# Performance work log

Hardware: AMD Instinct MI355X
Metric: run time of the kernel (lower is better)

The kernel has to match this reference:

```python
import jax, jax.numpy as jnp
import numpy as np

N_NODES = 100000
N_EDGES = 3200000
N_GRAPHS = 1000
IN_DIM = 10
HIDDEN = 64
N_CLASSES = 2


def setup_inputs() -> dict:
    key = jax.random.key(0)
    ks = jax.random.split(key, 12)
    x = jax.random.normal(ks[0], (N_NODES, IN_DIM), dtype=jnp.float32)
    edge_index = jax.random.randint(ks[1], (2, N_EDGES), 0, N_NODES, dtype=jnp.int64)
    batch = jnp.sort(jax.random.randint(ks[2], (N_NODES,), 0, N_GRAPHS, dtype=jnp.int64))
    def glorot(k, shape):
        lim = float(np.sqrt(6.0 / (shape[0] + shape[1])))
        return jax.random.uniform(k, shape, jnp.float32, -lim, lim)
    W1 = glorot(ks[3], (IN_DIM, HIDDEN)); b1 = jnp.zeros((HIDDEN,), jnp.float32)
    W2 = glorot(ks[4], (HIDDEN, HIDDEN)); b2 = jnp.zeros((HIDDEN,), jnp.float32)
    W3 = glorot(ks[5], (HIDDEN, HIDDEN)); b3 = jnp.zeros((HIDDEN,), jnp.float32)
    Wl = glorot(ks[6], (HIDDEN, N_CLASSES))
    bl = jnp.zeros((N_CLASSES,), jnp.float32)
    return {"x": x, "edge_index": edge_index, "batch": batch,
            "W1": W1, "b1": b1, "W2": W2, "b2": b2, "W3": W3, "b3": b3,
            "Wl": Wl, "bl": bl}


def _gcn_norm(edge_index, n_nodes):
    # PyG gcn_norm with add_self_loops=False: deg computed at target (col)
    row, col = edge_index[0], edge_index[1]
    deg = jax.ops.segment_sum(jnp.ones((edge_index.shape[1],), jnp.float32), col,
                              num_segments=n_nodes)
    dinv = jnp.where(deg > 0, deg ** -0.5, 0.0)
    return dinv[row] * dinv[col]  # [E]


def _gcn_conv(h, W, b, row, col, norm, n_nodes):
    h = h @ W                      # [N, H]
    msg = h[row] * norm[:, None]   # [E, H] gather + edge scale
    agg = jax.ops.segment_sum(msg, col, num_segments=n_nodes)  # scatter-add at target
    return agg + b


def reference(x, edge_index, batch, W1, b1, W2, b2, W3, b3, Wl, bl):
    row, col = edge_index[0], edge_index[1]
    norm = _gcn_norm(edge_index, N_NODES)
    h = jax.nn.relu(_gcn_conv(x, W1, b1, row, col, norm, N_NODES))
    h = jax.nn.relu(_gcn_conv(h, W2, b2, row, col, norm, N_NODES))
    node_embs = _gcn_conv(h, W3, b3, row, col, norm, N_NODES)
    graph_emb = jax.ops.segment_sum(node_embs, batch, num_segments=N_GRAPHS)  # global_add_pool
    # dropout is identity in eval mode
    logits = graph_emb @ Wl + bl
    return jax.nn.softmax(logits, axis=1)
```

## Files before the change

### kernel.cpp

```cpp
#include <hip/hip_runtime.h>

#define N_NODES 100000
#define N_EDGES 3200000
#define N_GRAPHS 1000
#define IN_DIM 10
#define HIDDEN 64
#define NQUADS (N_NODES / 4)

#define NRANGES 8
#define RANGE_SIZE ((N_NODES + NRANGES - 1) / NRANGES)
#define CHUNK_EDGES 4096

#define LAYER_BLOCKS 2048

__global__ void k_deg(const int* __restrict__ col, int* __restrict__ deg) {
    int e = blockIdx.x * blockDim.x + threadIdx.x;
    if (e < N_EDGES) atomicAdd(&deg[col[e]], 1);
}

__global__ __launch_bounds__(1024) void k_scan_block(const int* __restrict__ deg,
                                                     int* __restrict__ offs,
                                                     int* __restrict__ bsums) {
    __shared__ int s[1024];
    int t = threadIdx.x;
    int i = blockIdx.x * 1024 + t;
    int v = (i < N_NODES) ? deg[i] : 0;
    s[t] = v;
    __syncthreads();
    for (int d = 1; d < 1024; d <<= 1) {
        int x = (t >= d) ? s[t - d] : 0;
        __syncthreads();
        s[t] += x;
        __syncthreads();
    }
    if (i < N_NODES) offs[i] = s[t] - v;
    if (t == 1023) bsums[blockIdx.x] = s[t];
}

__global__ __launch_bounds__(128) void k_scan_top(int* __restrict__ bsums, int nb) {
    __shared__ int s[128];
    int t = threadIdx.x;
    int v = (t < nb) ? bsums[t] : 0;
    s[t] = v;
    __syncthreads();
    for (int d = 1; d < 128; d <<= 1) {
        int x = (t >= d) ? s[t - d] : 0;
        __syncthreads();
        s[t] += x;
        __syncthreads();
    }
    if (t < nb) bsums[t] = s[t] - v;
}

__global__ __launch_bounds__(1024) void k_scan_add(int* __restrict__ offs,
                                                   const int* __restrict__ bsums) {
    int i = blockIdx.x * 1024 + threadIdx.x;
    if (i < N_NODES) offs[i] += bsums[blockIdx.x];
}

__global__ void k_dinv(const int* __restrict__ deg, float* __restrict__ dinv) {
    int n = blockIdx.x * blockDim.x + threadIdx.x;
    if (n < N_NODES) {
        int d = deg[n];
        dinv[n] = (d > 0) ? rsqrtf((float)d) : 0.f;
    }
}

__global__ __launch_bounds__(256) void k_fill(const int* __restrict__ row,
                                              const int* __restrict__ col,
                                              const int* __restrict__ offs,
                                              int* __restrict__ cursor,
                                              int* __restrict__ csr_src) {
    int range = blockIdx.x & (NRANGES - 1);
    int chunk = blockIdx.x >> 3;
    int lo = range * RANGE_SIZE;
    int hi = lo + RANGE_SIZE;
    int base = chunk * CHUNK_EDGES + threadIdx.x;
#pragma unroll
    for (int k = 0; k < CHUNK_EDGES / 256; ++k) {
        int e = base + k * 256;
        if (e < N_EDGES) {
            int c = col[e];
            int r = row[e];
            if (c >= lo && c < hi) {
                int p = atomicAdd(&cursor[c], 1);
                csr_src[offs[c] + p] = r;
            }
        }
    }
}

__global__ __launch_bounds__(256) void k_prex(const float* __restrict__ x,
                                              const float* __restrict__ dinv,
                                              float* __restrict__ xs16) {
    int i = blockIdx.x * blockDim.x + threadIdx.x;
    if (i >= (N_NODES + 1) * 16) return;
    int n = i >> 4, f = i & 15;
    float v = 0.f;
    if (n < N_NODES && f < IN_DIM) v = x[n * IN_DIM + f] * dinv[n];
    xs16[i] = v;
}

__global__ __launch_bounds__(256) void k_layer1(const float* __restrict__ xs16,
                                                const float* __restrict__ dinv,
                                                const int* __restrict__ offs,
                                                const int* __restrict__ deg,
                                                const int* __restrict__ csr_src,
                                                const float* __restrict__ W1,
                                                const float* __restrict__ b1,
                                                float* __restrict__ h1s) {
    int lane = threadIdx.x & 63;
    int f = lane & 15;
    int gbase = lane & 48;
    float W1reg[16];
#pragma unroll
    for (int k = 0; k < 16; ++k) W1reg[k] = (k < IN_DIM) ? W1[k * HIDDEN + lane] : 0.f;
    float b1reg = b1[lane];

    int wid = (blockIdx.x * 256 + threadIdx.x) >> 6;
    int nwaves = gridDim.x * 4;
    for (int quad = wid; quad < NQUADS; quad += nwaves) {
        int n = quad * 4 + (lane >> 4);
        int start = offs[n], dn = deg[n];
        int maxd = max(max(__shfl(dn, 0), __shfl(dn, 16)),
                       max(__shfl(dn, 32), __shfl(dn, 48)));
        float a = 0.f;
        for (int base = 0; base < maxd; base += 16) {
            int s = csr_src[start + base + f];
            s = (base + f < dn) ? s : N_NODES;
#pragma unroll
            for (int jj = 0; jj < 2; ++jj) {
                float v[8];
#pragma unroll
                for (int j = 0; j < 8; ++j) {
                    int sj = __shfl(s, gbase + jj * 8 + j);
                    v[j] = xs16[sj * 16 + f];
                }
#pragma unroll
                for (int j = 0; j < 8; ++j) a += v[j];
            }
        }
        a *= dinv[n];
#pragma unroll
        for (int g = 0; g < 4; ++g) {
            float acc = b1reg;
#pragma unroll
            for (int k = 0; k < 16; ++k) {
                acc += __shfl(a, g * 16 + k) * W1reg[k];
            }
            int ng = quad * 4 + g;
            h1s[ng * HIDDEN + lane] = fmaxf(acc, 0.f) * dinv[ng];
        }
    }
}

__global__ __launch_bounds__(256) void k_layer2(const float* __restrict__ hs,
                                                const float* __restrict__ dinv,
                                                const int* __restrict__ offs,
                                                const int* __restrict__ deg,
                                                const int* __restrict__ csr_src,
                                                const float* __restrict__ W,
                                                const float* __restrict__ b,
                                                float* __restrict__ houts) {
    __shared__ float4 sW4[HIDDEN][16];
    for (int i = threadIdx.x; i < HIDDEN * 16; i += 256) {
        int k = i >> 4, f = i & 15;
        sW4[k][f] = *(const float4*)&W[k * HIDDEN + f * 4];
    }
    __syncthreads();
    int lane = threadIdx.x & 63;
    int f = lane & 15;
    int gbase = lane & 48;
    float4 b4 = *(const float4*)&b[f * 4];

    int wid = (blockIdx.x * 256 + threadIdx.x) >> 6;
    int nwaves = gridDim.x * 4;
    for (int quad = wid; quad < NQUADS; quad += nwaves) {
        int n = quad * 4 + (lane >> 4);
        int start = offs[n], dn = deg[n];
        int maxd = max(max(__shfl(dn, 0), __shfl(dn, 16)),
                       max(__shfl(dn, 32), __shfl(dn, 48)));
        float4 acc = make_float4(0.f, 0.f, 0.f, 0.f);
        for (int base = 0; base < maxd; base += 16) {
            int s = csr_src[start + base + f];
            s = (base + f < dn) ? s : N_NODES;
#pragma unroll
            for (int jj = 0; jj < 2; ++jj) {
                float4 v[8];
#pragma unroll
                for (int j = 0; j < 8; ++j) {
                    int sj = __shfl(s, gbase + jj * 8 + j);
                    v[j] = *(const float4*)&hs[sj * HIDDEN + f * 4];
                }
#pragma unroll
                for (int j = 0; j < 8; ++j) {
                    acc.x += v[j].x; acc.y += v[j].y; acc.z += v[j].z; acc.w += v[j].w;
                }
            }
        }
        float di = dinv[n];
        acc.x *= di; acc.y *= di; acc.z *= di; acc.w *= di;
        float4 out = b4;
#pragma unroll
        for (int k = 0; k < HIDDEN; ++k) {
            float srcval = (k & 3) == 0 ? acc.x : (k & 3) == 1 ? acc.y : (k & 3) == 2 ? acc.z : acc.w;
            float ak = __shfl(srcval, gbase + (k >> 2));
            float4 w4 = sW4[k][f];
            out.x += ak * w4.x; out.y += ak * w4.y; out.z += ak * w4.z; out.w += ak * w4.w;
        }
        out.x = fmaxf(out.x, 0.f) * di;
        out.y = fmaxf(out.y, 0.f) * di;
        out.z = fmaxf(out.z, 0.f) * di;
        out.w = fmaxf(out.w, 0.f) * di;
        *(float4*)&houts[n * HIDDEN + f * 4] = out;
    }
}

__global__ __launch_bounds__(256) void k_layer3(const float* __restrict__ hs,
                                                const float* __restrict__ dinv,
                                                const int* __restrict__ offs,
                                                const int* __restrict__ deg,
                                                const int* __restrict__ csr_src,
                                                const int* __restrict__ batch,
                                                float* __restrict__ gpre,
                                                int* __restrict__ gcnt) {
    int lane = threadIdx.x & 63;
    int f = lane & 15;
    int gbase = lane & 48;
    int wid = (blockIdx.x * 256 + threadIdx.x) >> 6;
    int nwaves = gridDim.x * 4;
    for (int quad = wid; quad < NQUADS; quad += nwaves) {
        int n = quad * 4 + (lane >> 4);
        int start = offs[n], dn = deg[n];
        int maxd = max(max(__shfl(dn, 0), __shfl(dn, 16)),
                       max(__shfl(dn, 32), __shfl(dn, 48)));
        float4 acc = make_float4(0.f, 0.f, 0.f, 0.f);
        for (int base = 0; base < maxd; base += 16) {
            int s = csr_src[start + base + f];
            s = (base + f < dn) ? s : N_NODES;
#pragma unroll
            for (int jj = 0; jj < 2; ++jj) {
                float4 v[8];
#pragma unroll
                for (int j = 0; j < 8; ++j) {
                    int sj = __shfl(s, gbase + jj * 8 + j);
                    v[j] = *(const float4*)&hs[sj * HIDDEN + f * 4];
                }
#pragma unroll
                for (int j = 0; j < 8; ++j) {
                    acc.x += v[j].x; acc.y += v[j].y; acc.z += v[j].z; acc.w += v[j].w;
                }
            }
        }
        float di = dinv[n];
        int g = batch[n];
        float* dst = &gpre[g * HIDDEN + f * 4];
        atomicAdd(dst + 0, acc.x * di);
        atomicAdd(dst + 1, acc.y * di);
        atomicAdd(dst + 2, acc.z * di);
        atomicAdd(dst + 3, acc.w * di);
        if (f == 0) atomicAdd(&gcnt[g], 1);
    }
}

__global__ __launch_bounds__(256) void k_final(const float* __restrict__ gpre,
                                               const int* __restrict__ gcnt,
                                               const float* __restrict__ W3,
                                               const float* __restrict__ b3,
                                               const float* __restrict__ Wl,
                                               const float* __restrict__ bl,
                                               float* __restrict__ out) {
    int wid = (blockIdx.x * blockDim.x + threadIdx.x) >> 6;
    int lane = threadIdx.x & 63;
    if (wid >= N_GRAPHS) return;
    float pre = gpre[wid * HIDDEN + lane];
    float cnt = (float)gcnt[wid];
    float emb = cnt * b3[lane];
    for (int k = 0; k < HIDDEN; ++k) {
        emb += __shfl(pre, k) * W3[k * HIDDEN + lane];
    }
    float p0 = emb * Wl[lane * 2 + 0];
    float p1 = emb * Wl[lane * 2 + 1];
    for (int d = 32; d > 0; d >>= 1) {
        p0 += __shfl_xor(p0, d);
        p1 += __shfl_xor(p1, d);
    }
    if (lane == 0) {
        float l0 = p0 + bl[0], l1 = p1 + bl[1];
        float m = fmaxf(l0, l1);
        float e0 = __expf(l0 - m), e1 = __expf(l1 - m);
        float inv = 1.f / (e0 + e1);
        out[wid * 2 + 0] = e0 * inv;
        out[wid * 2 + 1] = e1 * inv;
    }
}

extern "C" void kernel_launch(void* const* d_in, const int* in_sizes, int n_in,
                              void* d_out, int out_size, void* d_ws, size_t ws_size,
                              hipStream_t stream) {
    const float* x = (const float*)d_in[0];
    const int* edge = (const int*)d_in[1];
    const int* batch = (const int*)d_in[2];
    const float* W1 = (const float*)d_in[3];
    const float* b1 = (const float*)d_in[4];
    const float* W2 = (const float*)d_in[5];
    const float* b2 = (const float*)d_in[6];
    const float* W3 = (const float*)d_in[7];
    const float* b3 = (const float*)d_in[8];
    const float* Wl = (const float*)d_in[9];
    const float* bl = (const float*)d_in[10];
    float* out = (float*)d_out;

    const int* row = edge;
    const int* col = edge + N_EDGES;

    char* ws = (char*)d_ws;
    size_t off = 0;
    auto alloc = [&](size_t bytes) -> void* {
        void* p = ws + off;
        off = (off + bytes + 255) & ~(size_t)255;
        return p;
    };
    int* deg = (int*)alloc((size_t)N_NODES * 4);
    int* offs = (int*)alloc((size_t)N_NODES * 4);
    int* bsums = (int*)alloc(128 * 4);
    int* cursor = (int*)alloc((size_t)N_NODES * 4);
    float* dinv = (float*)alloc((size_t)N_NODES * 4);
    int* csr_src = (int*)alloc(((size_t)N_EDGES + 256) * 4);
    float* xs16 = (float*)alloc((size_t)(N_NODES + 1) * 16 * 4);
    float* h1s = (float*)alloc((size_t)(N_NODES + 1) * HIDDEN * 4);
    float* h2s = (float*)alloc((size_t)(N_NODES + 1) * HIDDEN * 4);
    float* gpre = (float*)alloc((size_t)N_GRAPHS * HIDDEN * 4);
    int* gcnt = (int*)alloc((size_t)N_GRAPHS * 4);

    hipMemsetAsync(deg, 0, (size_t)N_NODES * 4, stream);
    hipMemsetAsync(cursor, 0, (size_t)N_NODES * 4, stream);
    hipMemsetAsync(gpre, 0, (size_t)N_GRAPHS * HIDDEN * 4, stream);
    hipMemsetAsync(gcnt, 0, (size_t)N_GRAPHS * 4, stream);
    hipMemsetAsync(h1s + (size_t)N_NODES * HIDDEN, 0, HIDDEN * 4, stream);
    hipMemsetAsync(h2s + (size_t)N_NODES * HIDDEN, 0, HIDDEN * 4, stream);

    const int EB = (N_EDGES + 255) / 256;
    const int NB1024 = (N_NODES + 1023) / 1024;

    k_deg<<<EB, 256, 0, stream>>>(col, deg);
    k_scan_block<<<NB1024, 1024, 0, stream>>>(deg, offs, bsums);
    k_scan_top<<<1, 128, 0, stream>>>(bsums, NB1024);
    k_scan_add<<<NB1024, 1024, 0, stream>>>(offs, bsums);
    k_dinv<<<(N_NODES + 255) / 256, 256, 0, stream>>>(deg, dinv);

    const int NCHUNKS = (N_EDGES + CHUNK_EDGES - 1) / CHUNK_EDGES;
    k_fill<<<NCHUNKS * NRANGES, 256, 0, stream>>>(row, col, offs, cursor, csr_src);
    k_prex<<<((N_NODES + 1) * 16 + 255) / 256, 256, 0, stream>>>(x, dinv, xs16);

    k_layer1<<<LAYER_BLOCKS, 256, 0, stream>>>(xs16, dinv, offs, deg, csr_src, W1, b1, h1s);
    k_layer2<<<LAYER_BLOCKS, 256, 0, stream>>>(h1s, dinv, offs, deg, csr_src, W2, b2, h2s);
    k_layer3<<<LAYER_BLOCKS, 256, 0, stream>>>(h2s, dinv, offs, deg, csr_src, batch, gpre, gcnt);
    k_final<<<(N_GRAPHS * 64 + 255) / 256, 256, 0, stream>>>(gpre, gcnt, W3, b3, Wl, bl, out);
}
```

Measured before the change: 820.9 us.

## Split GCN layers into feature-sliced gather passes plus dense kernels

Stores node features in 8-wide feature slices (SoA of 8-float slabs) so each gather pass reads a 3.2MB table that can stay cache-resident, running one gather pass per slice, then separate dense transform kernels. Pooling replaces float atomics with per-graph contiguous range sums using min/max bounds from the sorted batch. This trades fused single-pass aggregation for more passes over the CSR index (8x reread) in exchange for better L2/MALL locality on random gathers.

```diff
diff --git a/kernel.cpp b/kernel.cpp
--- a/kernel.cpp
+++ b/kernel.cpp
@@ -1,6 +1,7 @@
 #include <hip/hip_runtime.h>
 
 #define N_NODES 100000
+#define N1 (N_NODES + 1)
 #define N_EDGES 3200000
 #define N_GRAPHS 1000
 #define IN_DIM 10
@@ -11,7 +12,8 @@
 #define RANGE_SIZE ((N_NODES + NRANGES - 1) / NRANGES)
 #define CHUNK_EDGES 4096
 
-#define LAYER_BLOCKS 2048
+#define SLICE (N1 * 8)
+#define GNB ((N_NODES + 3) / 4)
 
 __global__ void k_deg(const int* __restrict__ col, int* __restrict__ deg) {
     int e = blockIdx.x * blockDim.x + threadIdx.x;
@@ -90,115 +92,114 @@
     }
 }
 
-__global__ __launch_bounds__(256) void k_prex(const float* __restrict__ x,
-                                              const float* __restrict__ dinv,
-                                              float* __restrict__ xs16) {
+__global__ void k_prex(const float* __restrict__ x, const float* __restrict__ dinv,
+                       float* __restrict__ xsAB) {
     int i = blockIdx.x * blockDim.x + threadIdx.x;
-    if (i >= (N_NODES + 1) * 16) return;
-    int n = i >> 4, f = i & 15;
+    if (i >= N1 * 16) return;
+    int n = i >> 4, d = i & 15;
     float v = 0.f;
-    if (n < N_NODES && f < IN_DIM) v = x[n * IN_DIM + f] * dinv[n];
-    xs16[i] = v;
-}
-
-__global__ __launch_bounds__(256) void k_layer1(const float* __restrict__ xs16,
+    if (n < N_NODES && d < IN_DIM) v = x[n * IN_DIM + d] * dinv[n];
+    xsAB[(d >> 3) * SLICE + n * 8 + (d & 7)] = v;
+}
+
+__global__ void k_zerosink(float* __restrict__ hslc) {
+    int t = threadIdx.x;
+    hslc[(t >> 3) * SLICE + N_NODES * 8 + (t & 7)] = 0.f;
+}
+
+__global__ void k_bounds(const int* __restrict__ batch, int* __restrict__ gmin,
+                         int* __restrict__ gmax) {
+    int n = blockIdx.x * blockDim.x + threadIdx.x;
+    if (n < N_NODES) {
+        int g = batch[n];
+        atomicMin(&gmin[g], n);
+        atomicMax(&gmax[g], n + 1);
+    }
+}
+
+__global__ __launch_bounds__(256) void k_gather8(const float* __restrict__ tab0,
+                                                 const int* __restrict__ offs,
+                                                 const int* __restrict__ deg,
+                                                 const int* __restrict__ csr,
+                                                 float* __restrict__ out0) {
+    int pass = blockIdx.x / GNB;
+    int nb = blockIdx.x - pass * GNB;
+    const float* tab = tab0 + pass * SLICE;
+    float* outp = out0 + pass * SLICE;
+    int lane = threadIdx.x & 63;
+    int eg = lane >> 3, f = lane & 7;
+    int n = nb * 4 + (threadIdx.x >> 6);
+    if (n >= N_NODES) return;
+    int start = offs[n], dn = deg[n];
+    float acc = 0.f;
+    for (int base = 0; base < dn; base += 64) {
+        int raw = __builtin_nontemporal_load(&csr[start + base + lane]);
+        int idx = (base + lane < dn) ? raw : N_NODES;
+        float v[8];
+#pragma unroll
+        for (int t = 0; t < 8; ++t) {
+            int sj = __shfl(idx, t * 8 + eg);
+            v[t] = tab[sj * 8 + f];
+        }
+#pragma unroll
+        for (int t = 0; t < 8; ++t) acc += v[t];
+    }
+    acc += __shfl_xor(acc, 8);
+    acc += __shfl_xor(acc, 16);
+    acc += __shfl_xor(acc, 32);
+    if (lane < 8) outp[n * 8 + lane] = acc;
+}
+
+__global__ __launch_bounds__(256) void k_dense1(const float* __restrict__ agg,
                                                 const float* __restrict__ dinv,
-                                                const int* __restrict__ offs,
-                                                const int* __restrict__ deg,
-                                                const int* __restrict__ csr_src,
                                                 const float* __restrict__ W1,
                                                 const float* __restrict__ b1,
-                                                float* __restrict__ h1s) {
+                                                float* __restrict__ h1slc) {
     int lane = threadIdx.x & 63;
-    int f = lane & 15;
-    int gbase = lane & 48;
+    int f16 = lane & 15;
     float W1reg[16];
 #pragma unroll
     for (int k = 0; k < 16; ++k) W1reg[k] = (k < IN_DIM) ? W1[k * HIDDEN + lane] : 0.f;
     float b1reg = b1[lane];
-
+    int so = (lane >> 3) * SLICE + (lane & 7);
+    int ain = (f16 >> 3) * SLICE + (f16 & 7);
     int wid = (blockIdx.x * 256 + threadIdx.x) >> 6;
     int nwaves = gridDim.x * 4;
     for (int quad = wid; quad < NQUADS; quad += nwaves) {
         int n = quad * 4 + (lane >> 4);
-        int start = offs[n], dn = deg[n];
-        int maxd = max(max(__shfl(dn, 0), __shfl(dn, 16)),
-                       max(__shfl(dn, 32), __shfl(dn, 48)));
-        float a = 0.f;
-        for (int base = 0; base < maxd; base += 16) {
-            int s = csr_src[start + base + f];
-            s = (base + f < dn) ? s : N_NODES;
-#pragma unroll
-            for (int jj = 0; jj < 2; ++jj) {
-                float v[8];
-#pragma unroll
-                for (int j = 0; j < 8; ++j) {
-                    int sj = __shfl(s, gbase + jj * 8 + j);
-                    v[j] = xs16[sj * 16 + f];
-                }
-#pragma unroll
-                for (int j = 0; j < 8; ++j) a += v[j];
-            }
-        }
-        a *= dinv[n];
+        float a = agg[ain + n * 8] * dinv[n];
 #pragma unroll
         for (int g = 0; g < 4; ++g) {
             float acc = b1reg;
 #pragma unroll
-            for (int k = 0; k < 16; ++k) {
-                acc += __shfl(a, g * 16 + k) * W1reg[k];
-            }
+            for (int k = 0; k < 16; ++k) acc += __shfl(a, g * 16 + k) * W1reg[k];
             int ng = quad * 4 + g;
-            h1s[ng * HIDDEN + lane] = fmaxf(acc, 0.f) * dinv[ng];
+            h1slc[so + ng * 8] = fmaxf(acc, 0.f) * dinv[ng];
         }
     }
 }
 
-__global__ __launch_bounds__(256) void k_layer2(const float* __restrict__ hs,
+__global__ __launch_bounds__(256) void k_dense2(const float* __restrict__ agg,
                                                 const float* __restrict__ dinv,
-                                                const int* __restrict__ offs,
-                                                const int* __restrict__ deg,
-                                                const int* __restrict__ csr_src,
                                                 const float* __restrict__ W,
                                                 const float* __restrict__ b,
-                                                float* __restrict__ houts) {
+                                                float* __restrict__ outslc) {
     __shared__ float4 sW4[HIDDEN][16];
     for (int i = threadIdx.x; i < HIDDEN * 16; i += 256) {
-        int k = i >> 4, f = i & 15;
-        sW4[k][f] = *(const float4*)&W[k * HIDDEN + f * 4];
+        int k = i >> 4, ff = i & 15;
+        sW4[k][ff] = *(const float4*)&W[k * HIDDEN + ff * 4];
     }
     __syncthreads();
     int lane = threadIdx.x & 63;
-    int f = lane & 15;
-    int gbase = lane & 48;
+    int f = lane & 15, gbase = lane & 48;
     float4 b4 = *(const float4*)&b[f * 4];
-
+    int aoff = (f >> 1) * SLICE + (f & 1) * 4;
     int wid = (blockIdx.x * 256 + threadIdx.x) >> 6;
     int nwaves = gridDim.x * 4;
     for (int quad = wid; quad < NQUADS; quad += nwaves) {
         int n = quad * 4 + (lane >> 4);
-        int start = offs[n], dn = deg[n];
-        int maxd = max(max(__shfl(dn, 0), __shfl(dn, 16)),
-                       max(__shfl(dn, 32), __shfl(dn, 48)));
-        float4 acc = make_float4(0.f, 0.f, 0.f, 0.f);
-        for (int base = 0; base < maxd; base += 16) {
-            int s = csr_src[start + base + f];
-            s = (base + f < dn) ? s : N_NODES;
-#pragma unroll
-            for (int jj = 0; jj < 2; ++jj) {
-                float4 v[8];
-#pragma unroll
-                for (int j = 0; j < 8; ++j) {
-                    int sj = __shfl(s, gbase + jj * 8 + j);
-                    v[j] = *(const float4*)&hs[sj * HIDDEN + f * 4];
-                }
-#pragma unroll
-                for (int j = 0; j < 8; ++j) {
-                    acc.x += v[j].x; acc.y += v[j].y; acc.z += v[j].z; acc.w += v[j].w;
-                }
-            }
-        }
         float di = dinv[n];
+        float4 acc = *(const float4*)&agg[aoff + n * 8];
         acc.x *= di; acc.y *= di; acc.z *= di; acc.w *= di;
         float4 out = b4;
 #pragma unroll
@@ -212,58 +213,27 @@
         out.y = fmaxf(out.y, 0.f) * di;
         out.z = fmaxf(out.z, 0.f) * di;
         out.w = fmaxf(out.w, 0.f) * di;
-        *(float4*)&houts[n * HIDDEN + f * 4] = out;
-    }
-}
-
-__global__ __launch_bounds__(256) void k_layer3(const float* __restrict__ hs,
-                                                const float* __restrict__ dinv,
-                                                const int* __restrict__ offs,
-                                                const int* __restrict__ deg,
-                                                const int* __restrict__ csr_src,
-                                                const int* __restrict__ batch,
-                                                float* __restrict__ gpre,
-                                                int* __restrict__ gcnt) {
-    int lane = threadIdx.x & 63;
-    int f = lane & 15;
-    int gbase = lane & 48;
-    int wid = (blockIdx.x * 256 + threadIdx.x) >> 6;
-    int nwaves = gridDim.x * 4;
-    for (int quad = wid; quad < NQUADS; quad += nwaves) {
-        int n = quad * 4 + (lane >> 4);
-        int start = offs[n], dn = deg[n];
-        int maxd = max(max(__shfl(dn, 0), __shfl(dn, 16)),
-                       max(__shfl(dn, 32), __shfl(dn, 48)));
-        float4 acc = make_float4(0.f, 0.f, 0.f, 0.f);
-        for (int base = 0; base < maxd; base += 16) {
-            int s = csr_src[start + base + f];
-            s = (base + f < dn) ? s : N_NODES;
-#pragma unroll
-            for (int jj = 0; jj < 2; ++jj) {
-                float4 v[8];
-#pragma unroll
-                for (int j = 0; j < 8; ++j) {
-                    int sj = __shfl(s, gbase + jj * 8 + j);
-                    v[j] = *(const float4*)&hs[sj * HIDDEN + f * 4];
-                }
-#pragma unroll
-                for (int j = 0; j < 8; ++j) {
-                    acc.x += v[j].x; acc.y += v[j].y; acc.z += v[j].z; acc.w += v[j].w;
-                }
-            }
-        }
-        float di = dinv[n];
-        int g = batch[n];
-        float* dst = &gpre[g * HIDDEN + f * 4];
-        atomicAdd(dst + 0, acc.x * di);
-        atomicAdd(dst + 1, acc.y * di);
-        atomicAdd(dst + 2, acc.z * di);
-        atomicAdd(dst + 3, acc.w * di);
-        if (f == 0) atomicAdd(&gcnt[g], 1);
-    }
-}
-
-__global__ __launch_bounds__(256) void k_final(const float* __restrict__ gpre,
+        *(float4*)&outslc[aoff + n * 8] = out;
+    }
+}
+
+__global__ __launch_bounds__(64) void k_pool(const float* __restrict__ agg,
+                                             const float* __restrict__ dinv,
+                                             const int* __restrict__ gmin,
+                                             const int* __restrict__ gmax,
+                                             float* __restrict__ gpool,
+                                             int* __restrict__ gcnt) {
+    int g = blockIdx.x;
+    int d = threadIdx.x;
+    int off = (d >> 3) * SLICE + (d & 7);
+    int lo = gmin[g], hi = gmax[g];
+    float s = 0.f;
+    for (int n = lo; n < hi; ++n) s += agg[off + n * 8] * dinv[n];
+    gpool[g * HIDDEN + d] = s;
+    if (d == 0) gcnt[g] = (hi > lo) ? (hi - lo) : 0;
+}
+
+__global__ __launch_bounds__(256) void k_final(const float* __restrict__ gpool,
                                                const int* __restrict__ gcnt,
                                                const float* __restrict__ W3,
                                                const float* __restrict__ b3,
@@ -273,7 +243,7 @@
     int wid = (blockIdx.x * blockDim.x + threadIdx.x) >> 6;
     int lane = threadIdx.x & 63;
     if (wid >= N_GRAPHS) return;
-    float pre = gpre[wid * HIDDEN + lane];
+    float pre = gpool[wid * HIDDEN + lane];
     float cnt = (float)gcnt[wid];
     float emb = cnt * b3[lane];
     for (int k = 0; k < HIDDEN; ++k) {
@@ -327,18 +297,18 @@
     int* cursor = (int*)alloc((size_t)N_NODES * 4);
     float* dinv = (float*)alloc((size_t)N_NODES * 4);
     int* csr_src = (int*)alloc(((size_t)N_EDGES + 256) * 4);
-    float* xs16 = (float*)alloc((size_t)(N_NODES + 1) * 16 * 4);
-    float* h1s = (float*)alloc((size_t)(N_NODES + 1) * HIDDEN * 4);
-    float* h2s = (float*)alloc((size_t)(N_NODES + 1) * HIDDEN * 4);
-    float* gpre = (float*)alloc((size_t)N_GRAPHS * HIDDEN * 4);
+    float* xsAB = (float*)alloc((size_t)2 * SLICE * 4);
+    float* h1slc = (float*)alloc((size_t)8 * SLICE * 4);
+    float* aggA = (float*)alloc((size_t)8 * SLICE * 4);
+    float* gpool = (float*)alloc((size_t)N_GRAPHS * HIDDEN * 4);
+    int* gmin = (int*)alloc((size_t)N_GRAPHS * 4);
+    int* gmax = (int*)alloc((size_t)N_GRAPHS * 4);
     int* gcnt = (int*)alloc((size_t)N_GRAPHS * 4);
 
     hipMemsetAsync(deg, 0, (size_t)N_NODES * 4, stream);
     hipMemsetAsync(cursor, 0, (size_t)N_NODES * 4, stream);
-    hipMemsetAsync(gpre, 0, (size_t)N_GRAPHS * HIDDEN * 4, stream);
-    hipMemsetAsync(gcnt, 0, (size_t)N_GRAPHS * 4, stream);
-    hipMemsetAsync(h1s + (size_t)N_NODES * HIDDEN, 0, HIDDEN * 4, stream);
-    hipMemsetAsync(h2s + (size_t)N_NODES * HIDDEN, 0, HIDDEN * 4, stream);
+    hipMemsetAsync(gmin, 0x7f, (size_t)N_GRAPHS * 4, stream);
+    hipMemsetAsync(gmax, 0, (size_t)N_GRAPHS * 4, stream);
 
     const int EB = (N_EDGES + 255) / 256;
     const int NB1024 = (N_NODES + 1023) / 1024;
@@ -351,10 +321,15 @@
 
     const int NCHUNKS = (N_EDGES + CHUNK_EDGES - 1) / CHUNK_EDGES;
     k_fill<<<NCHUNKS * NRANGES, 256, 0, stream>>>(row, col, offs, cursor, csr_src);
-    k_prex<<<((N_NODES + 1) * 16 + 255) / 256, 256, 0, stream>>>(x, dinv, xs16);
-
-    k_layer1<<<LAYER_BLOCKS, 256, 0, stream>>>(xs16, dinv, offs, deg, csr_src, W1, b1, h1s);
-    k_layer2<<<LAYER_BLOCKS, 256, 0, stream>>>(h1s, dinv, offs, deg, csr_src, W2, b2, h2s);
-    k_layer3<<<LAYER_BLOCKS, 256, 0, stream>>>(h2s, dinv, offs, deg, csr_src, batch, gpre, gcnt);
-    k_final<<<(N_GRAPHS * 64 + 255) / 256, 256, 0, stream>>>(gpre, gcnt, W3, b3, Wl, bl, out);
-}
+    k_prex<<<(N1 * 16 + 255) / 256, 256, 0, stream>>>(x, dinv, xsAB);
+    k_zerosink<<<1, 64, 0, stream>>>(h1slc);
+    k_bounds<<<(N_NODES + 255) / 256, 256, 0, stream>>>(batch, gmin, gmax);
+
+    k_gather8<<<2 * GNB, 256, 0, stream>>>(xsAB, offs, deg, csr_src, aggA);
+    k_dense1<<<2048, 256, 0, stream>>>(aggA, dinv, W1, b1, h1slc);
+    k_gather8<<<8 * GNB, 256, 0, stream>>>(h1slc, offs, deg, csr_src, aggA);
+    k_dense2<<<2048, 256, 0, stream>>>(aggA, dinv, W2, b2, h1slc);
+    k_gather8<<<8 * GNB, 256, 0, stream>>>(h1slc, offs, deg, csr_src, aggA);
+    k_pool<<<N_GRAPHS, 64, 0, stream>>>(aggA, dinv, gmin, gmax, gpool, gcnt);
+    k_final<<<(N_GRAPHS * 64 + 255) / 256, 256, 0, stream>>>(gpool, gcnt, W3, b3, Wl, bl, out);
+}
```

Measured after the change: 1.077 ms. +31.2%, slower.
